# Performance work log

Hardware: AMD Instinct MI355X
Metric: run time of the kernel (lower is better)

## Reference

```python
import jax, jax.numpy as jnp
import numpy as np

K = 16  # top-k affinities kept per current-frame pixel (init arg k)


def setup_inputs() -> dict:
    key = jax.random.key(0)
    k1, k2 = jax.random.split(key)
    B, C, H, W = 2, 256, 64, 64
    N = H * W
    cur_prev_aff = jax.random.normal(k1, (B, N, N), dtype=jnp.float32)
    feat = jax.random.normal(k2, (B, C, H, W), dtype=jnp.float32)
    return {"cur_prev_aff": cur_prev_aff, "feat": feat}


def reference(cur_prev_aff, feat):
    # cur_prev_aff: [B, N, N] affinity from each current pixel i to each prev pixel j
    # feat:         [B, C, H, W] previous-frame features, N = H*W
    B, C, H, W = feat.shape
    N = H * W
    # top-k affinity masking per current pixel
    vals, idx = jax.lax.top_k(cur_prev_aff, K)      # [B, N, K]
    w = jax.nn.softmax(vals, axis=-1)               # normalized masked affinities (masked_cpa)
    # gather prev-frame features at top-k locations and weighted-sum
    feat_t = feat.reshape(B, C, N).transpose(0, 2, 1)        # [B, N, C]
    gathered = jax.vmap(lambda f, ix: f[ix])(feat_t, idx)    # [B, N, K, C]
    out = jnp.einsum('bnk,bnkc->bnc', w, gathered)           # [B, N, C]
    return out.transpose(0, 2, 1).reshape(B, C, H, W)
```

## Files before the change

kernel.cpp:

```cpp
#include <hip/hip_runtime.h>

#define N_PIX 4096
#define N_CH 256
#define KSEL 16
#define SCAP 64

__device__ __forceinline__ unsigned f2key(float f) {
  unsigned u = __float_as_uint(f);
  return u ^ ((unsigned)((int)u >> 31) | 0x80000000u);
}
__device__ __forceinline__ float key2f(unsigned k) {
  unsigned u = (k & 0x80000000u) ? (k ^ 0x80000000u) : ~k;
  return __uint_as_float(u);
}
__device__ __forceinline__ unsigned umax2(unsigned a, unsigned b) { return a > b ? a : b; }

__global__ void transpose_feat_kernel(const float* __restrict__ feat,
                                      float* __restrict__ feat_t) {
  __shared__ float tile[32][33];
  const int b = blockIdx.z;
  const int n0 = blockIdx.x * 32;
  const int c0 = blockIdx.y * 32;
  const int tx = threadIdx.x, ty = threadIdx.y;
  const float* src = feat + (size_t)b * N_CH * N_PIX;
  float* dst = feat_t + (size_t)b * N_PIX * N_CH;
#pragma unroll
  for (int j = 0; j < 32; j += 8)
    tile[ty + j][tx] = src[(size_t)(c0 + ty + j) * N_PIX + n0 + tx];
  __syncthreads();
#pragma unroll
  for (int j = 0; j < 32; j += 8)
    dst[(size_t)(n0 + ty + j) * N_CH + c0 + tx] = tile[tx][ty + j];
}

template <bool FT>
__global__ __launch_bounds__(256, 4) void topk_pk_kernel(
    const float* __restrict__ aff, const float* __restrict__ feat,
    float* __restrict__ out) {
  __shared__ unsigned s_slab[4][SCAP];
  __shared__ uint2 s_wj[4][KSEL];
  __shared__ float s_out[4][N_CH];

  const int tid = threadIdx.x;
  const int lane = tid & 63;
  const int w = tid >> 6;
  const int bid = blockIdx.x;
  const int rg = (bid & 7) * 256 + (bid >> 3);
  const int b = rg >> 10;
  const int i0 = (rg & 1023) * 4;
  const int row = rg * 4 + w;
  const unsigned long long lt = (1ull << lane) - 1ull;

  const float* arow_f = aff + (size_t)row * N_PIX;
  const float4* arow = (const float4*)arow_f;

  unsigned ph[32];
  unsigned m = 0;
  float4 fvA[4], fvB[4];
#pragma unroll
  for (int r = 0; r < 4; ++r) fvA[r] = arow[r * 64 + lane];
#pragma unroll
  for (int bq = 0; bq < 4; ++bq) {
    if (bq < 3) {
#pragma unroll
      for (int r = 0; r < 4; ++r)
        fvB[r] = arow[((bq + 1) * 4 + r) * 64 + lane];
    }
#pragma unroll
    for (int r = 0; r < 4; ++r) {
      const int q = bq * 4 + r;
      const float4 v = fvA[r];
      const unsigned k0 = f2key(v.x), k1 = f2key(v.y);
      const unsigned k2 = f2key(v.z), k3 = f2key(v.w);
      m = umax2(m, umax2(umax2(k0, k1), umax2(k2, k3)));
      ph[2 * q + 0] = (k1 & 0xFFFF0000u) | (k0 >> 16);
      ph[2 * q + 1] = (k3 & 0xFFFF0000u) | (k2 >> 16);
    }
#pragma unroll
    for (int r = 0; r < 4; ++r) fvA[r] = fvB[r];
  }

  const unsigned t = m >> 16;
  unsigned p1 = 0, need1 = KSEL;
#pragma unroll
  for (int bit = 15; bit >= 0; --bit) {
    const unsigned want = (p1 << 1) | 1u;
    const unsigned cnt = (unsigned)__popcll(__ballot((t >> bit) == want));
    const bool take = cnt >= need1;
    p1 = want - (take ? 0u : 1u);
    need1 = take ? need1 : need1 - cnt;
  }
  const unsigned T1 = p1;

  s_slab[w][lane] = 0xFFFFFFFFu;

  unsigned cl = 0, j0 = 0, j1 = 0, j2 = 0, j3 = 0;
#pragma unroll
  for (int p = 0; p < 32; ++p) {
    const unsigned lo = ph[p] & 0xFFFFu;
    const unsigned hi = ph[p] >> 16;
    const unsigned jlo = (unsigned)((p >> 1) * 256 + lane * 4 + (p & 1) * 2);
    if (lo >= T1) {
      j3 = (cl == 3) ? jlo : j3; j2 = (cl == 2) ? jlo : j2;
      j1 = (cl == 1) ? jlo : j1; j0 = (cl == 0) ? jlo : j0;
      ++cl;
    }
    if (hi >= T1) {
      const unsigned jhi = jlo + 1;
      j3 = (cl == 3) ? jhi : j3; j2 = (cl == 2) ? jhi : j2;
      j1 = (cl == 1) ? jhi : j1; j0 = (cl == 0) ? jhi : j0;
      ++cl;
    }
  }

  unsigned total;
  if (__builtin_expect(__ballot(cl > 4) == 0ull, 1)) {
    const unsigned long long c0m = __ballot(cl & 1u);
    const unsigned long long c1m = __ballot(cl & 2u);
    const unsigned long long c2m = __ballot(cl & 4u);
    const unsigned start = (unsigned)__popcll(c0m & lt) +
                           2u * (unsigned)__popcll(c1m & lt) +
                           4u * (unsigned)__popcll(c2m & lt);
    total = (unsigned)__popcll(c0m) + 2u * (unsigned)__popcll(c1m) +
            4u * (unsigned)__popcll(c2m);
    if (cl > 0 && start + 0 < SCAP) s_slab[w][start + 0] = j0;
    if (cl > 1 && start + 1 < SCAP) s_slab[w][start + 1] = j1;
    if (cl > 2 && start + 2 < SCAP) s_slab[w][start + 2] = j2;
    if (cl > 3 && start + 3 < SCAP) s_slab[w][start + 3] = j3;
  } else {
    unsigned base = 0;
#pragma unroll
    for (int p = 0; p < 32; ++p) {
      const unsigned lo = ph[p] & 0xFFFFu;
      const unsigned hi = ph[p] >> 16;
      const unsigned jlo = (unsigned)((p >> 1) * 256 + lane * 4 + (p & 1) * 2);
      {
        const bool sel = lo >= T1;
        const unsigned long long mk = __ballot(sel);
        if (sel) {
          const unsigned pos = base + (unsigned)__popcll(mk & lt);
          if (pos < SCAP) s_slab[w][pos] = jlo;
        }
        base += (unsigned)__popcll(mk);
      }
      {
        const bool sel = hi >= T1;
        const unsigned long long mk = __ballot(sel);
        if (sel) {
          const unsigned pos = base + (unsigned)__popcll(mk & lt);
          if (pos < SCAP) s_slab[w][pos] = jlo + 1;
        }
        base += (unsigned)__popcll(mk);
      }
    }
    total = base;
  }

  if (__builtin_expect(total <= SCAP, 1)) {
    const unsigned jj = s_slab[w][lane];
    const bool valid = jj != 0xFFFFFFFFu;
    const float fval = arow_f[valid ? jj : 0u];
    const unsigned cv = valid ? f2key(fval) : 0u;
    const unsigned cj = valid ? jj : 0xFFFFFFFFu;

    unsigned p2 = 0, need2 = KSEL;
    bool early = false;
    int bit = 31;
    for (; bit >= 0; --bit) {
      const unsigned want = (p2 << 1) | 1u;
      const unsigned cnt = (unsigned)__popcll(__ballot((cv >> bit) == want));
      if (cnt >= need2) {
        p2 = want;
        if (cnt == need2) { early = true; break; }
      } else {
        need2 -= cnt;
        p2 <<= 1;
      }
    }
    bool win;
    float vref;
    if (early) {
      const unsigned thr2 = p2 << bit;
      win = cv >= thr2;
      vref = key2f(thr2);
    } else {
      win = cv > p2;
      vref = key2f(p2);
      bool tq = (cv == p2) && valid;
      for (unsigned q = 0; q < need2; ++q) {
        unsigned mi = tq ? cj : 0xFFFFFFFFu;
#pragma unroll
        for (int off = 32; off; off >>= 1) {
          const unsigned o = (unsigned)__shfl_xor((int)mi, off, 64);
          mi = o < mi ? o : mi;
        }
        if (tq && cj == mi) { win = true; tq = false; }
      }
    }
    const unsigned long long wm = __ballot(win);
    if (win) {
      const unsigned rk = (unsigned)__popcll(wm & lt);
      s_wj[w][rk] = make_uint2(__float_as_uint(__expf(key2f(cv) - vref)), cj);
    }
  } else {
    unsigned p2 = 0, need2 = KSEL;
    for (int bit = 31; bit >= 0; --bit) {
      const unsigned want = (p2 << 1) | 1u;
      unsigned cnt = 0;
      for (int q = 0; q < 16; ++q) {
        float4 v = arow[q * 64 + lane];
        cnt += (unsigned)__popcll(__ballot((f2key(v.x) >> bit) == want));
        cnt += (unsigned)__popcll(__ballot((f2key(v.y) >> bit) == want));
        cnt += (unsigned)__popcll(__ballot((f2key(v.z) >> bit) == want));
        cnt += (unsigned)__popcll(__ballot((f2key(v.w) >> bit) == want));
      }
      const bool take = cnt >= need2;
      p2 = want - (take ? 0u : 1u);
      need2 = take ? need2 : need2 - cnt;
    }
    const float vref = key2f(p2);
    unsigned rk = 0;
    for (int q = 0; q < 16; ++q) {
      float4 v = arow[q * 64 + lane];
      const float fvv[4] = {v.x, v.y, v.z, v.w};
      for (int c = 0; c < 4; ++c) {
        const unsigned kk = f2key(fvv[c]);
        const bool sel = kk > p2;
        const unsigned long long mk = __ballot(sel);
        if (sel) {
          const unsigned pos = rk + (unsigned)__popcll(mk & lt);
          if (pos < KSEL)
            s_wj[w][pos] = make_uint2(__float_as_uint(__expf(fvv[c] - vref)),
                                      (unsigned)(q * 256 + lane * 4 + c));
        }
        rk += (unsigned)__popcll(mk);
      }
    }
    unsigned jprev = 0xFFFFFFFFu;
    for (unsigned tq = rk; tq < KSEL; ++tq) {
      unsigned mi = 0xFFFFFFFFu;
      for (int q = 0; q < 16; ++q) {
        float4 v = arow[q * 64 + lane];
        const float fvv[4] = {v.x, v.y, v.z, v.w};
        for (int c = 0; c < 4; ++c) {
          const unsigned j = (unsigned)(q * 256 + lane * 4 + c);
          if (f2key(fvv[c]) == p2 && (jprev == 0xFFFFFFFFu || j > jprev) && j < mi)
            mi = j;
        }
      }
#pragma unroll
      for (int off = 32; off; off >>= 1) {
        const unsigned o = (unsigned)__shfl_xor((int)mi, off, 64);
        mi = o < mi ? o : mi;
      }
      if (lane == 0) s_wj[w][tq] = make_uint2(__float_as_uint(1.0f), mi);
      jprev = mi;
    }
  }

  float ssum = 0.f;
#pragma unroll
  for (int k = 0; k < KSEL; ++k) ssum += __uint_as_float(s_wj[w][k].x);
  const float inv = 1.0f / ssum;

  float ax = 0.f, ay = 0.f, az = 0.f, aw2 = 0.f;
  if (FT) {
    const float* fb = feat + (size_t)b * N_PIX * N_CH + lane * 4;
#pragma unroll
    for (int k = 0; k < KSEL; ++k) {
      const uint2 tt = s_wj[w][k];
      const float ew = __uint_as_float(tt.x);
      const float4 f = *(const float4*)(fb + (size_t)tt.y * N_CH);
      ax += ew * f.x; ay += ew * f.y; az += ew * f.z; aw2 += ew * f.w;
    }
  } else {
    const float* fb = feat + (size_t)b * N_CH * N_PIX;
    const int c0s = lane * 4;
#pragma unroll
    for (int k = 0; k < KSEL; ++k) {
      const uint2 tt = s_wj[w][k];
      const float ew = __uint_as_float(tt.x);
      ax += ew * fb[(size_t)(c0s + 0) * N_PIX + tt.y];
      ay += ew * fb[(size_t)(c0s + 1) * N_PIX + tt.y];
      az += ew * fb[(size_t)(c0s + 2) * N_PIX + tt.y];
      aw2 += ew * fb[(size_t)(c0s + 3) * N_PIX + tt.y];
    }
  }
  float4 accv;
  accv.x = ax * inv; accv.y = ay * inv; accv.z = az * inv; accv.w = aw2 * inv;
  *(float4*)&s_out[w][lane * 4] = accv;

  __syncthreads();

  {
    const int c = tid;
    float4 o;
    o.x = s_out[0][c]; o.y = s_out[1][c]; o.z = s_out[2][c]; o.w = s_out[3][c];
    *(float4*)(out + ((size_t)(b * N_CH + c)) * N_PIX + i0) = o;
  }
}

extern "C" void kernel_launch(void* const* d_in, const int* in_sizes, int n_in,
                              void* d_out, int out_size, void* d_ws, size_t ws_size,
                              hipStream_t stream) {
  const float* aff = (const float*)d_in[0];
  const float* feat = (const float*)d_in[1];
  float* out = (float*)d_out;
  const size_t feat_t_bytes = (size_t)2 * N_PIX * N_CH * sizeof(float);
  if (ws_size >= feat_t_bytes) {
    float* feat_t = (float*)d_ws;
    dim3 tb(32, 8, 1);
    dim3 tg(N_PIX / 32, N_CH / 32, 2);
    transpose_feat_kernel<<<tg, tb, 0, stream>>>(feat, feat_t);
    topk_pk_kernel<true><<<2048, 256, 0, stream>>>(aff, feat_t, out);
  } else {
    topk_pk_kernel<false><<<2048, 256, 0, stream>>>(aff, feat, out);
  }
}
```

Measured before the change: 51.99 us.

## Process two affinity rows per wavefront with interleaved top-k selection

Each wavefront now handles two rows at once. Their loads, radix-threshold ballots and gathers are interleaved to expose more instruction-level and memory-level parallelism, and the grid is halved to 1024 blocks with 8 rows each. The second-pass radix select is made branch-free and fully unrolled, using a tie-count check instead of an early exit. The softmax sum is folded into the gather loop. Register pressure roughly doubles (launch bounds drop from 4 to 3 blocks), which may reduce occupancy or cause spills.

```diff
diff --git a/kernel.cpp b/kernel.cpp
--- a/kernel.cpp
+++ b/kernel.cpp
@@ -34,269 +34,400 @@
 }
 
 template <bool FT>
-__global__ __launch_bounds__(256, 4) void topk_pk_kernel(
+__global__ __launch_bounds__(256, 3) void topk_dual_kernel(
     const float* __restrict__ aff, const float* __restrict__ feat,
     float* __restrict__ out) {
-  __shared__ unsigned s_slab[4][SCAP];
-  __shared__ uint2 s_wj[4][KSEL];
-  __shared__ float s_out[4][N_CH];
+  __shared__ unsigned s_slab[4][2][SCAP];
+  __shared__ uint2 s_wj[4][2][KSEL];
+  __shared__ float s_out[8][N_CH];
 
   const int tid = threadIdx.x;
   const int lane = tid & 63;
   const int w = tid >> 6;
   const int bid = blockIdx.x;
-  const int rg = (bid & 7) * 256 + (bid >> 3);
-  const int b = rg >> 10;
-  const int i0 = (rg & 1023) * 4;
-  const int row = rg * 4 + w;
+  const int rg = (bid & 7) * 128 + (bid >> 3);
+  const int b = rg >> 9;
+  const int i0 = (rg & 511) * 8;
+  const int rowA = rg * 8 + 2 * w;
+  const int rowB = rowA + 1;
   const unsigned long long lt = (1ull << lane) - 1ull;
 
-  const float* arow_f = aff + (size_t)row * N_PIX;
-  const float4* arow = (const float4*)arow_f;
-
-  unsigned ph[32];
-  unsigned m = 0;
-  float4 fvA[4], fvB[4];
-#pragma unroll
-  for (int r = 0; r < 4; ++r) fvA[r] = arow[r * 64 + lane];
+  const float* arowA_f = aff + (size_t)rowA * N_PIX;
+  const float* arowB_f = aff + (size_t)rowB * N_PIX;
+  const float4* arowA = (const float4*)arowA_f;
+  const float4* arowB = (const float4*)arowB_f;
+
+  unsigned* const slabA = s_slab[w][0];
+  unsigned* const slabB = s_slab[w][1];
+  uint2* const wjA = s_wj[w][0];
+  uint2* const wjB = s_wj[w][1];
+
+  unsigned phA[32], phB[32];
+  unsigned mA = 0, mB = 0;
+  float4 bA[4], bB[4];
+#pragma unroll
+  for (int r = 0; r < 4; ++r) bA[r] = arowA[r * 64 + lane];
+#pragma unroll
+  for (int r = 0; r < 4; ++r) bB[r] = arowB[r * 64 + lane];
 #pragma unroll
   for (int bq = 0; bq < 4; ++bq) {
-    if (bq < 3) {
-#pragma unroll
-      for (int r = 0; r < 4; ++r)
-        fvB[r] = arow[((bq + 1) * 4 + r) * 64 + lane];
-    }
 #pragma unroll
     for (int r = 0; r < 4; ++r) {
       const int q = bq * 4 + r;
-      const float4 v = fvA[r];
+      const float4 v = bA[r];
       const unsigned k0 = f2key(v.x), k1 = f2key(v.y);
       const unsigned k2 = f2key(v.z), k3 = f2key(v.w);
-      m = umax2(m, umax2(umax2(k0, k1), umax2(k2, k3)));
-      ph[2 * q + 0] = (k1 & 0xFFFF0000u) | (k0 >> 16);
-      ph[2 * q + 1] = (k3 & 0xFFFF0000u) | (k2 >> 16);
-    }
-#pragma unroll
-    for (int r = 0; r < 4; ++r) fvA[r] = fvB[r];
-  }
-
-  const unsigned t = m >> 16;
-  unsigned p1 = 0, need1 = KSEL;
+      mA = umax2(mA, umax2(umax2(k0, k1), umax2(k2, k3)));
+      phA[2 * q + 0] = (k1 & 0xFFFF0000u) | (k0 >> 16);
+      phA[2 * q + 1] = (k3 & 0xFFFF0000u) | (k2 >> 16);
+    }
+    if (bq < 3) {
+#pragma unroll
+      for (int r = 0; r < 4; ++r) bA[r] = arowA[((bq + 1) * 4 + r) * 64 + lane];
+    }
+#pragma unroll
+    for (int r = 0; r < 4; ++r) {
+      const int q = bq * 4 + r;
+      const float4 v = bB[r];
+      const unsigned k0 = f2key(v.x), k1 = f2key(v.y);
+      const unsigned k2 = f2key(v.z), k3 = f2key(v.w);
+      mB = umax2(mB, umax2(umax2(k0, k1), umax2(k2, k3)));
+      phB[2 * q + 0] = (k1 & 0xFFFF0000u) | (k0 >> 16);
+      phB[2 * q + 1] = (k3 & 0xFFFF0000u) | (k2 >> 16);
+    }
+    if (bq < 3) {
+#pragma unroll
+      for (int r = 0; r < 4; ++r) bB[r] = arowB[((bq + 1) * 4 + r) * 64 + lane];
+    }
+  }
+
+  const unsigned tA = mA >> 16, tB = mB >> 16;
+  unsigned p1A = 0, need1A = KSEL, p1B = 0, need1B = KSEL;
 #pragma unroll
   for (int bit = 15; bit >= 0; --bit) {
-    const unsigned want = (p1 << 1) | 1u;
-    const unsigned cnt = (unsigned)__popcll(__ballot((t >> bit) == want));
-    const bool take = cnt >= need1;
-    p1 = want - (take ? 0u : 1u);
-    need1 = take ? need1 : need1 - cnt;
-  }
-  const unsigned T1 = p1;
-
-  s_slab[w][lane] = 0xFFFFFFFFu;
-
-  unsigned cl = 0, j0 = 0, j1 = 0, j2 = 0, j3 = 0;
+    const unsigned wantA = (p1A << 1) | 1u;
+    const unsigned cntA = (unsigned)__popcll(__ballot((tA >> bit) == wantA));
+    const unsigned wantB = (p1B << 1) | 1u;
+    const unsigned cntB = (unsigned)__popcll(__ballot((tB >> bit) == wantB));
+    const bool takeA = cntA >= need1A;
+    p1A = wantA - (takeA ? 0u : 1u);
+    need1A = takeA ? need1A : need1A - cntA;
+    const bool takeB = cntB >= need1B;
+    p1B = wantB - (takeB ? 0u : 1u);
+    need1B = takeB ? need1B : need1B - cntB;
+  }
+  const unsigned T1A = p1A, T1B = p1B;
+
+  slabA[lane] = 0xFFFFFFFFu;
+  slabB[lane] = 0xFFFFFFFFu;
+
+  unsigned clA = 0, a0 = 0, a1 = 0, a2 = 0, a3 = 0;
 #pragma unroll
   for (int p = 0; p < 32; ++p) {
-    const unsigned lo = ph[p] & 0xFFFFu;
-    const unsigned hi = ph[p] >> 16;
+    const unsigned lo = phA[p] & 0xFFFFu, hi = phA[p] >> 16;
     const unsigned jlo = (unsigned)((p >> 1) * 256 + lane * 4 + (p & 1) * 2);
-    if (lo >= T1) {
-      j3 = (cl == 3) ? jlo : j3; j2 = (cl == 2) ? jlo : j2;
-      j1 = (cl == 1) ? jlo : j1; j0 = (cl == 0) ? jlo : j0;
-      ++cl;
-    }
-    if (hi >= T1) {
+    if (lo >= T1A) {
+      a3 = (clA == 3) ? jlo : a3; a2 = (clA == 2) ? jlo : a2;
+      a1 = (clA == 1) ? jlo : a1; a0 = (clA == 0) ? jlo : a0;
+      ++clA;
+    }
+    if (hi >= T1A) {
       const unsigned jhi = jlo + 1;
-      j3 = (cl == 3) ? jhi : j3; j2 = (cl == 2) ? jhi : j2;
-      j1 = (cl == 1) ? jhi : j1; j0 = (cl == 0) ? jhi : j0;
-      ++cl;
-    }
-  }
-
-  unsigned total;
-  if (__builtin_expect(__ballot(cl > 4) == 0ull, 1)) {
-    const unsigned long long c0m = __ballot(cl & 1u);
-    const unsigned long long c1m = __ballot(cl & 2u);
-    const unsigned long long c2m = __ballot(cl & 4u);
+      a3 = (clA == 3) ? jhi : a3; a2 = (clA == 2) ? jhi : a2;
+      a1 = (clA == 1) ? jhi : a1; a0 = (clA == 0) ? jhi : a0;
+      ++clA;
+    }
+  }
+  unsigned clB = 0, b0r = 0, b1r = 0, b2r = 0, b3r = 0;
+#pragma unroll
+  for (int p = 0; p < 32; ++p) {
+    const unsigned lo = phB[p] & 0xFFFFu, hi = phB[p] >> 16;
+    const unsigned jlo = (unsigned)((p >> 1) * 256 + lane * 4 + (p & 1) * 2);
+    if (lo >= T1B) {
+      b3r = (clB == 3) ? jlo : b3r; b2r = (clB == 2) ? jlo : b2r;
+      b1r = (clB == 1) ? jlo : b1r; b0r = (clB == 0) ? jlo : b0r;
+      ++clB;
+    }
+    if (hi >= T1B) {
+      const unsigned jhi = jlo + 1;
+      b3r = (clB == 3) ? jhi : b3r; b2r = (clB == 2) ? jhi : b2r;
+      b1r = (clB == 1) ? jhi : b1r; b0r = (clB == 0) ? jhi : b0r;
+      ++clB;
+    }
+  }
+
+  unsigned totalA, totalB;
+  if (__builtin_expect(__ballot(clA > 4) == 0ull, 1)) {
+    const unsigned long long c0m = __ballot(clA & 1u);
+    const unsigned long long c1m = __ballot(clA & 2u);
+    const unsigned long long c2m = __ballot(clA & 4u);
     const unsigned start = (unsigned)__popcll(c0m & lt) +
                            2u * (unsigned)__popcll(c1m & lt) +
                            4u * (unsigned)__popcll(c2m & lt);
-    total = (unsigned)__popcll(c0m) + 2u * (unsigned)__popcll(c1m) +
-            4u * (unsigned)__popcll(c2m);
-    if (cl > 0 && start + 0 < SCAP) s_slab[w][start + 0] = j0;
-    if (cl > 1 && start + 1 < SCAP) s_slab[w][start + 1] = j1;
-    if (cl > 2 && start + 2 < SCAP) s_slab[w][start + 2] = j2;
-    if (cl > 3 && start + 3 < SCAP) s_slab[w][start + 3] = j3;
+    totalA = (unsigned)__popcll(c0m) + 2u * (unsigned)__popcll(c1m) +
+             4u * (unsigned)__popcll(c2m);
+    if (clA > 0 && start + 0 < SCAP) slabA[start + 0] = a0;
+    if (clA > 1 && start + 1 < SCAP) slabA[start + 1] = a1;
+    if (clA > 2 && start + 2 < SCAP) slabA[start + 2] = a2;
+    if (clA > 3 && start + 3 < SCAP) slabA[start + 3] = a3;
   } else {
     unsigned base = 0;
 #pragma unroll
     for (int p = 0; p < 32; ++p) {
-      const unsigned lo = ph[p] & 0xFFFFu;
-      const unsigned hi = ph[p] >> 16;
+      const unsigned lo = phA[p] & 0xFFFFu, hi = phA[p] >> 16;
       const unsigned jlo = (unsigned)((p >> 1) * 256 + lane * 4 + (p & 1) * 2);
       {
-        const bool sel = lo >= T1;
+        const bool sel = lo >= T1A;
         const unsigned long long mk = __ballot(sel);
         if (sel) {
           const unsigned pos = base + (unsigned)__popcll(mk & lt);
-          if (pos < SCAP) s_slab[w][pos] = jlo;
+          if (pos < SCAP) slabA[pos] = jlo;
         }
         base += (unsigned)__popcll(mk);
       }
       {
-        const bool sel = hi >= T1;
+        const bool sel = hi >= T1A;
         const unsigned long long mk = __ballot(sel);
         if (sel) {
           const unsigned pos = base + (unsigned)__popcll(mk & lt);
-          if (pos < SCAP) s_slab[w][pos] = jlo + 1;
+          if (pos < SCAP) slabA[pos] = jlo + 1;
         }
         base += (unsigned)__popcll(mk);
       }
     }
-    total = base;
-  }
-
-  if (__builtin_expect(total <= SCAP, 1)) {
-    const unsigned jj = s_slab[w][lane];
-    const bool valid = jj != 0xFFFFFFFFu;
-    const float fval = arow_f[valid ? jj : 0u];
-    const unsigned cv = valid ? f2key(fval) : 0u;
-    const unsigned cj = valid ? jj : 0xFFFFFFFFu;
-
-    unsigned p2 = 0, need2 = KSEL;
-    bool early = false;
-    int bit = 31;
-    for (; bit >= 0; --bit) {
-      const unsigned want = (p2 << 1) | 1u;
-      const unsigned cnt = (unsigned)__popcll(__ballot((cv >> bit) == want));
-      if (cnt >= need2) {
-        p2 = want;
-        if (cnt == need2) { early = true; break; }
-      } else {
-        need2 -= cnt;
-        p2 <<= 1;
-      }
-    }
-    bool win;
-    float vref;
-    if (early) {
-      const unsigned thr2 = p2 << bit;
-      win = cv >= thr2;
-      vref = key2f(thr2);
+    totalA = base;
+  }
+  if (__builtin_expect(__ballot(clB > 4) == 0ull, 1)) {
+    const unsigned long long c0m = __ballot(clB & 1u);
+    const unsigned long long c1m = __ballot(clB & 2u);
+    const unsigned long long c2m = __ballot(clB & 4u);
+    const unsigned start = (unsigned)__popcll(c0m & lt) +
+                           2u * (unsigned)__popcll(c1m & lt) +
+                           4u * (unsigned)__popcll(c2m & lt);
+    totalB = (unsigned)__popcll(c0m) + 2u * (unsigned)__popcll(c1m) +
+             4u * (unsigned)__popcll(c2m);
+    if (clB > 0 && start + 0 < SCAP) slabB[start + 0] = b0r;
+    if (clB > 1 && start + 1 < SCAP) slabB[start + 1] = b1r;
+    if (clB > 2 && start + 2 < SCAP) slabB[start + 2] = b2r;
+    if (clB > 3 && start + 3 < SCAP) slabB[start + 3] = b3r;
+  } else {
+    unsigned base = 0;
+#pragma unroll
+    for (int p = 0; p < 32; ++p) {
+      const unsigned lo = phB[p] & 0xFFFFu, hi = phB[p] >> 16;
+      const unsigned jlo = (unsigned)((p >> 1) * 256 + lane * 4 + (p & 1) * 2);
+      {
+        const bool sel = lo >= T1B;
+        const unsigned long long mk = __ballot(sel);
+        if (sel) {
+          const unsigned pos = base + (unsigned)__popcll(mk & lt);
+          if (pos < SCAP) slabB[pos] = jlo;
+        }
+        base += (unsigned)__popcll(mk);
+      }
+      {
+        const bool sel = hi >= T1B;
+        const unsigned long long mk = __ballot(sel);
+        if (sel) {
+          const unsigned pos = base + (unsigned)__popcll(mk & lt);
+          if (pos < SCAP) slabB[pos] = jlo + 1;
+        }
+        base += (unsigned)__popcll(mk);
+      }
+    }
+    totalB = base;
+  }
+
+  const bool okA = totalA <= SCAP, okB = totalB <= SCAP;
+  if (__builtin_expect(okA && okB, 1)) {
+    const unsigned jjA = slabA[lane];
+    const unsigned jjB = slabB[lane];
+    const bool validA = jjA != 0xFFFFFFFFu;
+    const bool validB = jjB != 0xFFFFFFFFu;
+    const float fvalA = arowA_f[validA ? jjA : 0u];
+    const float fvalB = arowB_f[validB ? jjB : 0u];
+    const unsigned cvA = validA ? f2key(fvalA) : 0u;
+    const unsigned cvB = validB ? f2key(fvalB) : 0u;
+    const unsigned cjA = validA ? jjA : 0xFFFFFFFFu;
+    const unsigned cjB = validB ? jjB : 0xFFFFFFFFu;
+
+    unsigned p2A = 0, need2A = KSEL, p2B = 0, need2B = KSEL;
+#pragma unroll
+    for (int bit = 31; bit >= 0; --bit) {
+      const unsigned wantA = (p2A << 1) | 1u;
+      const unsigned cntA = (unsigned)__popcll(__ballot((cvA >> bit) == wantA));
+      const unsigned wantB = (p2B << 1) | 1u;
+      const unsigned cntB = (unsigned)__popcll(__ballot((cvB >> bit) == wantB));
+      const bool takeA = cntA >= need2A;
+      p2A = wantA - (takeA ? 0u : 1u);
+      need2A = takeA ? need2A : need2A - cntA;
+      const bool takeB = cntB >= need2B;
+      p2B = wantB - (takeB ? 0u : 1u);
+      need2B = takeB ? need2B : need2B - cntB;
+    }
+    bool winA = cvA > p2A, winB = cvB > p2B;
+    const bool eqA = validA && (cvA == p2A);
+    const bool eqB = validB && (cvB == p2B);
+    const unsigned cntEqA = (unsigned)__popcll(__ballot(eqA));
+    const unsigned cntEqB = (unsigned)__popcll(__ballot(eqB));
+    if (__builtin_expect(cntEqA == need2A, 1)) {
+      winA = winA || eqA;
     } else {
-      win = cv > p2;
-      vref = key2f(p2);
-      bool tq = (cv == p2) && valid;
-      for (unsigned q = 0; q < need2; ++q) {
-        unsigned mi = tq ? cj : 0xFFFFFFFFu;
+      bool tq = eqA;
+      for (unsigned q = 0; q < need2A; ++q) {
+        unsigned mi = tq ? cjA : 0xFFFFFFFFu;
 #pragma unroll
         for (int off = 32; off; off >>= 1) {
           const unsigned o = (unsigned)__shfl_xor((int)mi, off, 64);
           mi = o < mi ? o : mi;
         }
-        if (tq && cj == mi) { win = true; tq = false; }
-      }
-    }
-    const unsigned long long wm = __ballot(win);
-    if (win) {
-      const unsigned rk = (unsigned)__popcll(wm & lt);
-      s_wj[w][rk] = make_uint2(__float_as_uint(__expf(key2f(cv) - vref)), cj);
-    }
+        if (tq && cjA == mi) { winA = true; tq = false; }
+      }
+    }
+    if (__builtin_expect(cntEqB == need2B, 1)) {
+      winB = winB || eqB;
+    } else {
+      bool tq = eqB;
+      for (unsigned q = 0; q < need2B; ++q) {
+        unsigned mi = tq ? cjB : 0xFFFFFFFFu;
+#pragma unroll
+        for (int off = 32; off; off >>= 1) {
+          const unsigned o = (unsigned)__shfl_xor((int)mi, off, 64);
+          mi = o < mi ? o : mi;
+        }
+        if (tq && cjB == mi) { winB = true; tq = false; }
+      }
+    }
+    const unsigned long long wmA = __ballot(winA);
+    const unsigned long long wmB = __ballot(winB);
+    if (winA)
+      wjA[(unsigned)__popcll(wmA & lt)] =
+          make_uint2(__float_as_uint(__expf(key2f(cvA) - key2f(p2A))), cjA);
+    if (winB)
+      wjB[(unsigned)__popcll(wmB & lt)] =
+          make_uint2(__float_as_uint(__expf(key2f(cvB) - key2f(p2B))), cjB);
   } else {
-    unsigned p2 = 0, need2 = KSEL;
-    for (int bit = 31; bit >= 0; --bit) {
-      const unsigned want = (p2 << 1) | 1u;
-      unsigned cnt = 0;
+#pragma unroll
+    for (int rr = 0; rr < 2; ++rr) {
+      const bool bad = rr == 0 ? !okA : !okB;
+      if (!bad) continue;
+      const float* arf = rr == 0 ? arowA_f : arowB_f;
+      const float4* ar4 = rr == 0 ? arowA : arowB;
+      uint2* wj = rr == 0 ? wjA : wjB;
+      unsigned p2 = 0, need2 = KSEL;
+      for (int bit = 31; bit >= 0; --bit) {
+        const unsigned want = (p2 << 1) | 1u;
+        unsigned cnt = 0;
+        for (int q = 0; q < 16; ++q) {
+          float4 v = ar4[q * 64 + lane];
+          cnt += (unsigned)__popcll(__ballot((f2key(v.x) >> bit) == want));
+          cnt += (unsigned)__popcll(__ballot((f2key(v.y) >> bit) == want));
+          cnt += (unsigned)__popcll(__ballot((f2key(v.z) >> bit) == want));
+          cnt += (unsigned)__popcll(__ballot((f2key(v.w) >> bit) == want));
+        }
+        const bool take = cnt >= need2;
+        p2 = want - (take ? 0u : 1u);
+        need2 = take ? need2 : need2 - cnt;
+      }
+      const float vref = key2f(p2);
+      unsigned rk = 0;
       for (int q = 0; q < 16; ++q) {
-        float4 v = arow[q * 64 + lane];
-        cnt += (unsigned)__popcll(__ballot((f2key(v.x) >> bit) == want));
-        cnt += (unsigned)__popcll(__ballot((f2key(v.y) >> bit) == want));
-        cnt += (unsigned)__popcll(__ballot((f2key(v.z) >> bit) == want));
-        cnt += (unsigned)__popcll(__ballot((f2key(v.w) >> bit) == want));
-      }
-      const bool take = cnt >= need2;
-      p2 = want - (take ? 0u : 1u);
-      need2 = take ? need2 : need2 - cnt;
-    }
-    const float vref = key2f(p2);
-    unsigned rk = 0;
-    for (int q = 0; q < 16; ++q) {
-      float4 v = arow[q * 64 + lane];
-      const float fvv[4] = {v.x, v.y, v.z, v.w};
-      for (int c = 0; c < 4; ++c) {
-        const unsigned kk = f2key(fvv[c]);
-        const bool sel = kk > p2;
-        const unsigned long long mk = __ballot(sel);
-        if (sel) {
-          const unsigned pos = rk + (unsigned)__popcll(mk & lt);
-          if (pos < KSEL)
-            s_wj[w][pos] = make_uint2(__float_as_uint(__expf(fvv[c] - vref)),
-                                      (unsigned)(q * 256 + lane * 4 + c));
-        }
-        rk += (unsigned)__popcll(mk);
-      }
-    }
-    unsigned jprev = 0xFFFFFFFFu;
-    for (unsigned tq = rk; tq < KSEL; ++tq) {
-      unsigned mi = 0xFFFFFFFFu;
-      for (int q = 0; q < 16; ++q) {
-        float4 v = arow[q * 64 + lane];
+        float4 v = ar4[q * 64 + lane];
         const float fvv[4] = {v.x, v.y, v.z, v.w};
         for (int c = 0; c < 4; ++c) {
-          const unsigned j = (unsigned)(q * 256 + lane * 4 + c);
-          if (f2key(fvv[c]) == p2 && (jprev == 0xFFFFFFFFu || j > jprev) && j < mi)
-            mi = j;
-        }
-      }
-#pragma unroll
-      for (int off = 32; off; off >>= 1) {
-        const unsigned o = (unsigned)__shfl_xor((int)mi, off, 64);
-        mi = o < mi ? o : mi;
-      }
-      if (lane == 0) s_wj[w][tq] = make_uint2(__float_as_uint(1.0f), mi);
-      jprev = mi;
-    }
-  }
-
-  float ssum = 0.f;
-#pragma unroll
-  for (int k = 0; k < KSEL; ++k) ssum += __uint_as_float(s_wj[w][k].x);
-  const float inv = 1.0f / ssum;
-
-  float ax = 0.f, ay = 0.f, az = 0.f, aw2 = 0.f;
+          const unsigned kk = f2key(fvv[c]);
+          const bool sel = kk > p2;
+          const unsigned long long mk = __ballot(sel);
+          if (sel) {
+            const unsigned pos = rk + (unsigned)__popcll(mk & lt);
+            if (pos < KSEL)
+              wj[pos] = make_uint2(__float_as_uint(__expf(fvv[c] - vref)),
+                                   (unsigned)(q * 256 + lane * 4 + c));
+          }
+          rk += (unsigned)__popcll(mk);
+        }
+      }
+      unsigned jprev = 0xFFFFFFFFu;
+      for (unsigned tq = rk; tq < KSEL; ++tq) {
+        unsigned mi = 0xFFFFFFFFu;
+        for (int q = 0; q < 16; ++q) {
+          float4 v = ar4[q * 64 + lane];
+          const float fvv[4] = {v.x, v.y, v.z, v.w};
+          for (int c = 0; c < 4; ++c) {
+            const unsigned j = (unsigned)(q * 256 + lane * 4 + c);
+            if (f2key(fvv[c]) == p2 && (jprev == 0xFFFFFFFFu || j > jprev) &&
+                j < mi)
+              mi = j;
+          }
+        }
+#pragma unroll
+        for (int off = 32; off; off >>= 1) {
+          const unsigned o = (unsigned)__shfl_xor((int)mi, off, 64);
+          mi = o < mi ? o : mi;
+        }
+        if (lane == 0) wj[tq] = make_uint2(__float_as_uint(1.0f), mi);
+        jprev = mi;
+      }
+      (void)arf;
+    }
+  }
+
+  float ssumA = 0.f, ssumB = 0.f;
+  float axA = 0.f, ayA = 0.f, azA = 0.f, awA = 0.f;
+  float axB = 0.f, ayB = 0.f, azB = 0.f, awB = 0.f;
   if (FT) {
     const float* fb = feat + (size_t)b * N_PIX * N_CH + lane * 4;
 #pragma unroll
     for (int k = 0; k < KSEL; ++k) {
-      const uint2 tt = s_wj[w][k];
-      const float ew = __uint_as_float(tt.x);
-      const float4 f = *(const float4*)(fb + (size_t)tt.y * N_CH);
-      ax += ew * f.x; ay += ew * f.y; az += ew * f.z; aw2 += ew * f.w;
+      const uint2 ttA = wjA[k];
+      const uint2 ttB = wjB[k];
+      const float ewA = __uint_as_float(ttA.x);
+      const float ewB = __uint_as_float(ttB.x);
+      ssumA += ewA; ssumB += ewB;
+      const float4 fA = *(const float4*)(fb + (size_t)ttA.y * N_CH);
+      const float4 fB = *(const float4*)(fb + (size_t)ttB.y * N_CH);
+      axA += ewA * fA.x; ayA += ewA * fA.y; azA += ewA * fA.z; awA += ewA * fA.w;
+      axB += ewB * fB.x; ayB += ewB * fB.y; azB += ewB * fB.z; awB += ewB * fB.w;
     }
   } else {
     const float* fb = feat + (size_t)b * N_CH * N_PIX;
     const int c0s = lane * 4;
 #pragma unroll
     for (int k = 0; k < KSEL; ++k) {
-      const uint2 tt = s_wj[w][k];
-      const float ew = __uint_as_float(tt.x);
-      ax += ew * fb[(size_t)(c0s + 0) * N_PIX + tt.y];
-      ay += ew * fb[(size_t)(c0s + 1) * N_PIX + tt.y];
-      az += ew * fb[(size_t)(c0s + 2) * N_PIX + tt.y];
-      aw2 += ew * fb[(size_t)(c0s + 3) * N_PIX + tt.y];
-    }
-  }
-  float4 accv;
-  accv.x = ax * inv; accv.y = ay * inv; accv.z = az * inv; accv.w = aw2 * inv;
-  *(float4*)&s_out[w][lane * 4] = accv;
+      const uint2 ttA = wjA[k];
+      const uint2 ttB = wjB[k];
+      const float ewA = __uint_as_float(ttA.x);
+      const float ewB = __uint_as_float(ttB.x);
+      ssumA += ewA; ssumB += ewB;
+#pragma unroll
+      for (int c = 0; c < 4; ++c) {
+        const float vA = fb[(size_t)(c0s + c) * N_PIX + ttA.y];
+        const float vB = fb[(size_t)(c0s + c) * N_PIX + ttB.y];
+        if (c == 0) { axA += ewA * vA; axB += ewB * vB; }
+        if (c == 1) { ayA += ewA * vA; ayB += ewB * vB; }
+        if (c == 2) { azA += ewA * vA; azB += ewB * vB; }
+        if (c == 3) { awA += ewA * vA; awB += ewB * vB; }
+      }
+    }
+  }
+  const float invA = 1.0f / ssumA;
+  const float invB = 1.0f / ssumB;
+  float4 oA, oB;
+  oA.x = axA * invA; oA.y = ayA * invA; oA.z = azA * invA; oA.w = awA * invA;
+  oB.x = axB * invB; oB.y = ayB * invB; oB.z = azB * invB; oB.w = awB * invB;
+  *(float4*)&s_out[2 * w + 0][lane * 4] = oA;
+  *(float4*)&s_out[2 * w + 1][lane * 4] = oB;
 
   __syncthreads();
 
   {
     const int c = tid;
-    float4 o;
-    o.x = s_out[0][c]; o.y = s_out[1][c]; o.z = s_out[2][c]; o.w = s_out[3][c];
-    *(float4*)(out + ((size_t)(b * N_CH + c)) * N_PIX + i0) = o;
+    float4 o1, o2;
+    o1.x = s_out[0][c]; o1.y = s_out[1][c]; o1.z = s_out[2][c]; o1.w = s_out[3][c];
+    o2.x = s_out[4][c]; o2.y = s_out[5][c]; o2.z = s_out[6][c]; o2.w = s_out[7][c];
+    float* op = out + ((size_t)(b * N_CH + c)) * N_PIX + i0;
+    *(float4*)op = o1;
+    *(float4*)(op + 4) = o2;
   }
 }
 
@@ -312,8 +443,8 @@
     dim3 tb(32, 8, 1);
     dim3 tg(N_PIX / 32, N_CH / 32, 2);
     transpose_feat_kernel<<<tg, tb, 0, stream>>>(feat, feat_t);
-    topk_pk_kernel<true><<<2048, 256, 0, stream>>>(aff, feat_t, out);
+    topk_dual_kernel<true><<<1024, 256, 0, stream>>>(aff, feat_t, out);
   } else {
-    topk_pk_kernel<false><<<2048, 256, 0, stream>>>(aff, feat, out);
+    topk_dual_kernel<false><<<1024, 256, 0, stream>>>(aff, feat, out);
   }
 }
```

Result: slower. 65.79 us (+26.5%).
